# Optimization experiments

Measured on AMD Instinct MI355X. Metric: run time of the kernel, lower is better.

The kernel has to match this reference:

```python
import jax, jax.numpy as jnp
import numpy as np

B, H, S, P = 4, 16, 1024, 64
D = H * P  # state_size = 1024


def setup_inputs() -> dict:
    key = jax.random.key(0)
    k0, k1, k2, k3, k4 = jax.random.split(key, 5)
    q = jax.random.normal(k0, (B * H, S, P), jnp.float32)
    k = jax.random.normal(k1, (B * H, S, P), jnp.float32)
    v = jax.random.normal(k2, (B * H, S, P), jnp.float32)
    # xavier_uniform for the merge projection (fan_in = fan_out = D)
    limit = np.sqrt(6.0 / (D + D)).astype(np.float32)
    w_merge = jax.random.uniform(k3, (D, D), jnp.float32, -limit, limit)
    # causal position mask: True = masked (as used by masked_fill)
    position_mask = jnp.triu(jnp.ones((S, S), dtype=bool), k=1)
    # source-length padding mask: True = padded position
    lengths = jax.random.randint(k4, (B,), S // 2, S + 1)
    src_length_mask = jnp.arange(S)[None, :] >= lengths[:, None]
    return {"q": q, "k": k, "v": v, "w_merge": w_merge,
            "position_mask": position_mask, "src_length_mask": src_length_mask}


def reference(q, k, v, w_merge, position_mask, src_length_mask):
    # q,k,v: [B*H, S, P]; position_mask: [S,S] bool; src_length_mask: [B,S] bool
    BH, T, Pp = q.shape
    nb = src_length_mask.shape[0]
    nh = BH // nb
    scale = 1.0 / np.sqrt(Pp).astype(np.float32)
    # logits = bmm(q, k^T) * scale
    logits = jnp.einsum('btp,bsp->bts', q, k) * scale  # [B*H, T, S]
    logits = logits.reshape(nb, nh, T, T)
    logits = jnp.where(position_mask[None, None, :, :], -jnp.inf, logits)
    logits = jnp.where(src_length_mask[:, None, None, :], -jnp.inf, logits)
    scores = jax.nn.softmax(logits, axis=-1).reshape(BH, T, T)
    # dropout is identity in eval / p=0
    data = jnp.einsum('bts,bsp->btp', scores, v)  # [B*H, T, P]
    # merge heads: [B, H, T, P] -> [B, T, H*P]
    data = data.reshape(nb, nh, T, Pp).transpose(0, 2, 1, 3).reshape(nb, T, nh * Pp)
    return data @ w_merge.T  # Linear(bias=False)
```

## Files before the change

kernel.cpp:

```cpp
#include <hip/hip_runtime.h>
#include <hip/hip_bf16.h>
#include <math.h>


typedef _Float16 f16x8 __attribute__((ext_vector_type(8)));
typedef unsigned short u16x8 __attribute__((ext_vector_type(8)));
typedef float f32x4 __attribute__((ext_vector_type(4)));
typedef float f32x16 __attribute__((ext_vector_type(16)));

union H8 { u16x8 u; f16x8 h; };
union PAF { unsigned int w[4]; f16x8 h; };

static __device__ __forceinline__ unsigned short f2hu(float f) {
  _Float16 h = (_Float16)f;
  unsigned short u;
  __builtin_memcpy(&u, &h, 2);
  return u;
}

static __device__ __forceinline__ unsigned int pk2(float lo, float hi) {
  auto t = __builtin_amdgcn_cvt_pkrtz(lo, hi);
  unsigned int u;
  __builtin_memcpy(&u, &t, 4);
  return u;
}

#define PLSWAP(a, b) asm("v_permlane32_swap_b32 %0, %1" : "+v"(a), "+v"(b))

#define MFMA16(a, b, c) __builtin_amdgcn_mfma_f32_16x16x32_f16((a), (b), (c), 0, 0, 0)
#define MFMA32(a, b, c) __builtin_amdgcn_mfma_f32_32x32x16_f16((a), (b), (c), 0, 0, 0)

static __device__ __forceinline__ void gload16(const void* g, void* l) {
  __builtin_amdgcn_global_load_lds(
      (const __attribute__((address_space(1))) unsigned int*)g,
      (__attribute__((address_space(3))) unsigned int*)l, 16, 0, 0);
}

__global__ __launch_bounds__(256) void prep_all(const float* __restrict__ w,
                                                const int* __restrict__ smask,
                                                const float* __restrict__ kin,
                                                const float* __restrict__ vin,
                                                unsigned short* __restrict__ w_sw,
                                                unsigned short* __restrict__ k_sw,
                                                unsigned short* __restrict__ v_sw,
                                                int* __restrict__ lengths) {
  const int bid = blockIdx.x;
  const int tid = threadIdx.x;
  if (bid < 4) {
    __shared__ int sh[256];
    int4 m = ((const int4*)(smask + bid * 1024))[tid];
    sh[tid] = (m.x != 0) + (m.y != 0) + (m.z != 0) + (m.w != 0);
    __syncthreads();
    for (int o = 128; o > 0; o >>= 1) {
      if (tid < o) sh[tid] += sh[tid + o];
      __syncthreads();
    }
    if (tid == 0) lengths[bid] = 1024 - sh[0];
  } else if (bid < 1028) {
    int idx = (bid - 4) * 256 + tid;
    float4 f = ((const float4*)w)[idx];
    ushort4 o;
    o.x = f2hu(f.x); o.y = f2hu(f.y); o.z = f2hu(f.z); o.w = f2hu(f.w);
    int row = idx >> 8;
    int c4 = (idx & 255) * 4;
    int nt = row >> 6, r = row & 63, kt = c4 >> 6, cb = (c4 & 63) * 2;
    *(ushort4*)((char*)w_sw + ((size_t)(nt * 16 + kt)) * 8192 +
                ((r * 128 + cb) ^ ((r & 7) << 4))) = o;
  } else if (bid < 3076) {
    int idx = (bid - 1028) * 256 + tid;
    const float4* src = ((const float4*)kin) + (size_t)idx * 2;
    float4 a = src[0], b = src[1];
    u16x8 o;
    o[0] = f2hu(a.x); o[1] = f2hu(a.y); o[2] = f2hu(a.z); o[3] = f2hu(a.w);
    o[4] = f2hu(b.x); o[5] = f2hu(b.y); o[6] = f2hu(b.z); o[7] = f2hu(b.w);
    int bh = idx >> 13;
    int i = idx & 8191;
    int s = i >> 3;
    int c16 = i & 7;
    int kt = s >> 6, r = s & 63;
    int xb = (r * 128 + c16 * 16) ^ ((r & 7) << 4);
    *(u16x8*)((char*)k_sw + ((size_t)(bh * 16 + kt)) * 8192 + xb) = o;
  } else {
    const int t = bid - 3076;
    const int bh = t >> 4;
    const int st = t & 15;
    __shared__ unsigned short T[64][72];
    const float* vp = vin + ((size_t)bh * 1024 + st * 64) * 64;
#pragma unroll
    for (int i = 0; i < 4; ++i) {
      int e = i * 256 + tid;
      int row = e >> 4;
      int c4 = (e & 15) * 4;
      float4 f = *(const float4*)(vp + row * 64 + c4);
      T[c4 + 0][row] = f2hu(f.x);
      T[c4 + 1][row] = f2hu(f.y);
      T[c4 + 2][row] = f2hu(f.z);
      T[c4 + 3][row] = f2hu(f.w);
    }
    __syncthreads();
#pragma unroll
    for (int i = 0; i < 4; ++i) {
      int e = i * 256 + tid;
      int feat = e >> 4;
      int c4 = (e & 15) * 4;
      ushort4 o;
      o.x = T[feat][c4 + 0]; o.y = T[feat][c4 + 1];
      o.z = T[feat][c4 + 2]; o.w = T[feat][c4 + 3];
      int xb = (feat * 128 + c4 * 2) ^ ((feat & 7) << 4);
      *(ushort4*)((char*)v_sw + ((size_t)(bh * 16 + st)) * 8192 + xb) = o;
    }
  }
}

static __device__ __forceinline__ void store_attn_sw(unsigned short* attn_sw,
                                                     int b, int hh, int trow,
                                                     int feat, float v) {
  int grow = b * 1024 + trow;
  int mt = grow >> 7, rr = grow & 127;
  int cb = feat * 2;
  *(unsigned short*)((char*)attn_sw + ((size_t)(mt * 16 + hh)) * 16384 +
                     ((rr * 128 + cb) ^ ((rr & 7) << 4))) = f2hu(v);
}

__global__ __launch_bounds__(256, 2) void attn_w32(const float* __restrict__ q,
                                                   const unsigned short* __restrict__ k_sw,
                                                   const unsigned short* __restrict__ v_sw,
                                                   const int* __restrict__ lengths,
                                                   unsigned short* __restrict__ attn_sw) {
  const int wg = blockIdx.x;
  const int idx = (wg & 7) * 64 + (wg >> 3);
  const int bh = idx >> 3;
  const int p = idx & 7;
  const int qtB = 15 - p;
  const int b = bh >> 4;
  const int hh = bh & 15;
  const int tid = threadIdx.x;
  const int lane = tid & 63;
  const int wv = tid >> 6;
  const int l31 = lane & 31;
  const int h = lane >> 5;
  const int len = lengths[b];

  const int selB = ((wv >> 1) ^ (wg & 1)) & 1;
  const int qt = selB ? qtB : p;
  const int qb = qt * 64 + (wv & 1) * 32;
  const int trow = qb + l31;

  const int lcap = (len - 1) >> 6;
  const int mynkt = ((lcap < qt) ? lcap : qt) + 1;
  const int nktB = ((lcap < qtB) ? lcap : qtB) + 1;

  __shared__ __align__(16) unsigned short Kb[3][4096];
  __shared__ __align__(16) unsigned short Vb[3][4096];

  const char* kbase_sw = (const char*)k_sw + (size_t)bh * 16 * 8192;
  const char* vbase_sw = (const char*)v_sw + (size_t)bh * 16 * 8192;

  H8 qf[4];
  {
    const float* qp = q + ((size_t)bh * 1024 + qb + l31) * 64;
#pragma unroll
    for (int c = 0; c < 4; ++c) {
      const float* p0 = qp + c * 16 + h * 8;
      float4 f0 = *(const float4*)(p0);
      float4 f1 = *(const float4*)(p0 + 4);
      u16x8 u;
      u[0] = f2hu(f0.x); u[1] = f2hu(f0.y); u[2] = f2hu(f0.z); u[3] = f2hu(f0.w);
      u[4] = f2hu(f1.x); u[5] = f2hu(f1.y); u[6] = f2hu(f1.z); u[7] = f2hu(f1.w);
      qf[c].u = u;
    }
  }

  f32x16 oacc0 = {}, oacc1 = {};
  float psum = 0.f;

#define STAGE_T(t, buf)                                                      \
  do {                                                                       \
    const char* ks_ = kbase_sw + (size_t)(t) * 8192;                         \
    const char* vs_ = vbase_sw + (size_t)(t) * 8192;                         \
    _Pragma("unroll") for (int j = 0; j < 2; ++j) {                          \
      int ch = wv * 2 + j;                                                   \
      gload16(ks_ + ch * 1024 + lane * 16, (char*)Kb[buf] + ch * 1024);      \
      gload16(vs_ + ch * 1024 + lane * 16, (char*)Vb[buf] + ch * 1024);      \
    }                                                                        \
  } while (0)

  STAGE_T(0, 0);
  STAGE_T(1, 1);

  for (int kt = 0; kt < nktB; ++kt) {
    const int cur = kt % 3;
    if (kt + 1 < nktB) {
      asm volatile("s_waitcnt vmcnt(4)" ::: "memory");
    } else {
      asm volatile("s_waitcnt vmcnt(0)" ::: "memory");
    }
    __builtin_amdgcn_s_barrier();
    if (kt + 2 < nktB) STAGE_T(kt + 2, (kt + 2) % 3);

    if (kt < mynkt) {
      const char* Kc = (const char*)Kb[cur];
      const char* Vc = (const char*)Vb[cur];

      f32x16 sacc0 = {}, sacc1 = {};
      __builtin_amdgcn_s_setprio(1);
#pragma unroll
      for (int c = 0; c < 4; ++c) {
        const int cb = c * 32 + h * 16;
        H8 kf0, kf1;
        kf0.u = *(const u16x8*)(Kc + ((l31 * 128 + cb) ^ ((l31 & 7) << 4)));
        const int r1 = 32 + l31;
        kf1.u = *(const u16x8*)(Kc + ((r1 * 128 + cb) ^ ((r1 & 7) << 4)));
        sacc0 = MFMA32(kf0.h, qf[c].h, sacc0);
        sacc1 = MFMA32(kf1.h, qf[c].h, sacc1);
      }
      __builtin_amdgcn_s_setprio(0);

      unsigned int paw[4][4];
      float ps = 0.f;
#pragma unroll
      for (int kb2 = 0; kb2 < 2; ++kb2) {
        float pv[16];
#pragma unroll
        for (int r = 0; r < 16; ++r) {
          float sv = kb2 ? sacc1[r] : sacc0[r];
          int srl = (r & 3) + 8 * (r >> 2) + 4 * h;
          int scol = kt * 64 + kb2 * 32 + srl;
          float e = __expf(fmaf(sv, 0.125f, -5.0f));
          pv[r] = (scol > trow || scol >= len) ? 0.f : e;
          ps += pv[r];
        }
        unsigned int X0 = pk2(pv[0], pv[1]), X1 = pk2(pv[2], pv[3]);
        unsigned int Y0 = pk2(pv[4], pv[5]), Y1 = pk2(pv[6], pv[7]);
        unsigned int Z0 = pk2(pv[8], pv[9]), Z1 = pk2(pv[10], pv[11]);
        unsigned int W0 = pk2(pv[12], pv[13]), W1 = pk2(pv[14], pv[15]);
        PLSWAP(X0, Y0);
        PLSWAP(X1, Y1);
        PLSWAP(Z0, W0);
        PLSWAP(Z1, W1);
        paw[kb2 * 2 + 0][0] = X0; paw[kb2 * 2 + 0][1] = X1;
        paw[kb2 * 2 + 0][2] = Y0; paw[kb2 * 2 + 0][3] = Y1;
        paw[kb2 * 2 + 1][0] = Z0; paw[kb2 * 2 + 1][1] = Z1;
        paw[kb2 * 2 + 1][2] = W0; paw[kb2 * 2 + 1][3] = W1;
      }
      psum += ps;

      __builtin_amdgcn_s_setprio(1);
#pragma unroll
      for (int c = 0; c < 4; ++c) {
        PAF pa;
        pa.w[0] = paw[c][0]; pa.w[1] = paw[c][1];
        pa.w[2] = paw[c][2]; pa.w[3] = paw[c][3];
        const int cb = c * 32 + h * 16;
        H8 vf0, vf1;
        vf0.u = *(const u16x8*)(Vc + ((l31 * 128 + cb) ^ ((l31 & 7) << 4)));
        const int r1 = 32 + l31;
        vf1.u = *(const u16x8*)(Vc + ((r1 * 128 + cb) ^ ((r1 & 7) << 4)));
        oacc0 = MFMA32(pa.h, vf0.h, oacc0);
        oacc1 = MFMA32(pa.h, vf1.h, oacc1);
      }
      __builtin_amdgcn_s_setprio(0);
    }
  }
#undef STAGE_T

  float sa = psum, sb = psum;
  PLSWAP(sa, sb);
  float inv = 1.0f / (sa + sb);
#pragma unroll
  for (int r = 0; r < 16; ++r) {
    int crow = (r & 3) + 8 * (r >> 2) + 4 * h;
    float invr = __int_as_float(
        __builtin_amdgcn_ds_bpermute(crow << 2, __float_as_int(inv)));
    int tr = qb + crow;
    store_attn_sw(attn_sw, b, hh, tr, l31, oacc0[r] * invr);
    store_attn_sw(attn_sw, b, hh, tr, 32 + l31, oacc1[r] * invr);
  }
}

__global__ __launch_bounds__(256, 2) void merge_sw(const unsigned short* __restrict__ a_sw,
                                                   const unsigned short* __restrict__ w_sw,
                                                   float* __restrict__ out) {
  const int mt = blockIdx.x;
  const int nt = blockIdx.y;
  const int tid = threadIdx.x;
  const int lane = tid & 63;
  const int wv = tid >> 6;
  const int l15 = lane & 15;
  const int kgrp = lane >> 4;
  const int wr = wv >> 1;
  const int wc = wv & 1;

  __shared__ __align__(16) unsigned short Ab[3][8192];
  __shared__ __align__(16) unsigned short Wb[3][4096];

  const char* abase = (const char*)a_sw + (size_t)mt * 16 * 16384;
  const char* wbase = (const char*)w_sw + (size_t)nt * 16 * 8192;

  f32x4 acc[4][2] = {};

#define MSTAGE(t, buf)                                                    \
  do {                                                                    \
    const char* as_ = abase + (size_t)(t) * 16384;                        \
    const char* ws_ = wbase + (size_t)(t) * 8192;                         \
    _Pragma("unroll") for (int j = 0; j < 4; ++j) {                       \
      int ch = wv * 4 + j;                                                \
      gload16(as_ + ch * 1024 + lane * 16, (char*)Ab[buf] + ch * 1024);   \
    }                                                                     \
    _Pragma("unroll") for (int j = 0; j < 2; ++j) {                       \
      int ch = wv * 2 + j;                                                \
      gload16(ws_ + ch * 1024 + lane * 16, (char*)Wb[buf] + ch * 1024);   \
    }                                                                     \
  } while (0)

  MSTAGE(0, 0);
  MSTAGE(1, 1);

  for (int t = 0; t < 16; ++t) {
    const int cur = t % 3;
    if (t + 1 < 16) {
      asm volatile("s_waitcnt vmcnt(6)" ::: "memory");
    } else {
      asm volatile("s_waitcnt vmcnt(0)" ::: "memory");
    }
    __builtin_amdgcn_s_barrier();
    if (t + 2 < 16) MSTAGE(t + 2, (t + 2) % 3);

    __builtin_amdgcn_s_setprio(1);
#pragma unroll
    for (int kb = 0; kb < 2; kb++) {
      H8 wf[2];
#pragma unroll
      for (int nb = 0; nb < 2; nb++) {
        int wrow = wc * 32 + nb * 16 + l15;
        wf[nb].u = *(const u16x8*)((const char*)Wb[cur] +
                    ((wrow * 128 + (kb * 32 + kgrp * 8) * 2) ^ ((wrow & 7) << 4)));
      }
#pragma unroll
      for (int mb = 0; mb < 4; mb++) {
        int arow = wr * 64 + mb * 16 + l15;
        H8 aa;
        aa.u = *(const u16x8*)((const char*)Ab[cur] +
                ((arow * 128 + (kb * 32 + kgrp * 8) * 2) ^ ((arow & 7) << 4)));
#pragma unroll
        for (int nb = 0; nb < 2; nb++)
          acc[mb][nb] = MFMA16(aa.h, wf[nb].h, acc[mb][nb]);
      }
    }
    __builtin_amdgcn_s_setprio(0);
  }
#undef MSTAGE

  const int m0 = mt * 128, n0 = nt * 64;
#pragma unroll
  for (int mb = 0; mb < 4; mb++)
#pragma unroll
    for (int nb = 0; nb < 2; nb++)
#pragma unroll
      for (int r = 0; r < 4; r++)
        out[(size_t)(m0 + wr * 64 + mb * 16 + kgrp * 4 + r) * 1024 +
            n0 + wc * 32 + nb * 16 + l15] = acc[mb][nb][r];
}

extern "C" void kernel_launch(void* const* d_in, const int* in_sizes, int n_in,
                              void* d_out, int out_size, void* d_ws, size_t ws_size,
                              hipStream_t stream) {
  const float* q = (const float*)d_in[0];
  const float* k = (const float*)d_in[1];
  const float* v = (const float*)d_in[2];
  const float* w = (const float*)d_in[3];
  const int* smask = (const int*)d_in[5];
  float* out = (float*)d_out;

  char* ws = (char*)d_ws;
  const size_t MB = 1024 * 1024;
  int* lengths = (int*)ws;
  unsigned short* w_sw = (unsigned short*)(ws + 256);
  unsigned short* attn_sw = (unsigned short*)(ws + 256 + 2 * MB);
  unsigned short* k_sw = (unsigned short*)(ws + 256 + 10 * MB);
  unsigned short* v_sw = (unsigned short*)(ws + 256 + 18 * MB);

  hipLaunchKernelGGL(prep_all, dim3(4100), dim3(256), 0, stream,
                     w, smask, k, v, w_sw, k_sw, v_sw, lengths);
  hipLaunchKernelGGL(attn_w32, dim3(512), dim3(256), 0, stream,
                     q, k_sw, v_sw, lengths, attn_sw);
  hipLaunchKernelGGL(merge_sw, dim3(32, 16), dim3(256), 0, stream, attn_sw, w_sw, out);
}
```

Measured before the change: 63.46 us.

## Replace LDS-staged attention with single-wave blocks reading K/V directly from global

Attention no longer stages K and V tiles into LDS through a triple-buffered async pipeline with barriers. It now launches one 64-thread wave per 32-row query block, and each wave reads K rows and transposed V straight from global memory in plain row-major fp16 layouts. The prep kernel writes K and V^T linearly instead of in swizzled tiles. This removes LDS traffic and barrier synchronisation, but loses K/V sharing across waves and the overlap of loads with compute, so it leans on L2 and cache hits and may stall on global load latency.

```diff
diff --git a/kernel.cpp b/kernel.cpp
--- a/kernel.cpp
+++ b/kernel.cpp
@@ -41,8 +41,8 @@
                                                 const float* __restrict__ kin,
                                                 const float* __restrict__ vin,
                                                 unsigned short* __restrict__ w_sw,
-                                                unsigned short* __restrict__ k_sw,
-                                                unsigned short* __restrict__ v_sw,
+                                                unsigned short* __restrict__ k_h,
+                                                unsigned short* __restrict__ vt_h,
                                                 int* __restrict__ lengths) {
   const int bid = blockIdx.x;
   const int tid = threadIdx.x;
@@ -73,13 +73,7 @@
     u16x8 o;
     o[0] = f2hu(a.x); o[1] = f2hu(a.y); o[2] = f2hu(a.z); o[3] = f2hu(a.w);
     o[4] = f2hu(b.x); o[5] = f2hu(b.y); o[6] = f2hu(b.z); o[7] = f2hu(b.w);
-    int bh = idx >> 13;
-    int i = idx & 8191;
-    int s = i >> 3;
-    int c16 = i & 7;
-    int kt = s >> 6, r = s & 63;
-    int xb = (r * 128 + c16 * 16) ^ ((r & 7) << 4);
-    *(u16x8*)((char*)k_sw + ((size_t)(bh * 16 + kt)) * 8192 + xb) = o;
+    ((u16x8*)k_h)[idx] = o;
   } else {
     const int t = bid - 3076;
     const int bh = t >> 4;
@@ -106,8 +100,7 @@
       ushort4 o;
       o.x = T[feat][c4 + 0]; o.y = T[feat][c4 + 1];
       o.z = T[feat][c4 + 2]; o.w = T[feat][c4 + 3];
-      int xb = (feat * 128 + c4 * 2) ^ ((feat & 7) << 4);
-      *(ushort4*)((char*)v_sw + ((size_t)(bh * 16 + st)) * 8192 + xb) = o;
+      *(ushort4*)(vt_h + ((size_t)bh * 64 + feat) * 1024 + st * 64 + c4) = o;
     }
   }
 }
@@ -122,39 +115,29 @@
                      ((rr * 128 + cb) ^ ((rr & 7) << 4))) = f2hu(v);
 }
 
-__global__ __launch_bounds__(256, 2) void attn_w32(const float* __restrict__ q,
-                                                   const unsigned short* __restrict__ k_sw,
-                                                   const unsigned short* __restrict__ v_sw,
-                                                   const int* __restrict__ lengths,
-                                                   unsigned short* __restrict__ attn_sw) {
-  const int wg = blockIdx.x;
-  const int idx = (wg & 7) * 64 + (wg >> 3);
-  const int bh = idx >> 3;
-  const int p = idx & 7;
-  const int qtB = 15 - p;
+__global__ __launch_bounds__(64, 2) void attn_direct(const float* __restrict__ q,
+                                                     const unsigned short* __restrict__ k_h,
+                                                     const unsigned short* __restrict__ vt_h,
+                                                     const int* __restrict__ lengths,
+                                                     unsigned short* __restrict__ attn_sw) {
+  const int w = blockIdx.x;
+  const int xcd = w & 7;
+  const int j = w >> 3;
+  const int bh = xcd * 8 + (j >> 5);
+  const int s = j & 31;
+  const int pp = s >> 1;
+  const int half = s & 1;
+  const int qt = (pp & 1) ? (pp >> 1) : (15 - (pp >> 1));
   const int b = bh >> 4;
   const int hh = bh & 15;
-  const int tid = threadIdx.x;
-  const int lane = tid & 63;
-  const int wv = tid >> 6;
+  const int lane = threadIdx.x;
   const int l31 = lane & 31;
   const int h = lane >> 5;
   const int len = lengths[b];
-
-  const int selB = ((wv >> 1) ^ (wg & 1)) & 1;
-  const int qt = selB ? qtB : p;
-  const int qb = qt * 64 + (wv & 1) * 32;
+  const int qb = qt * 64 + half * 32;
   const int trow = qb + l31;
-
   const int lcap = (len - 1) >> 6;
-  const int mynkt = ((lcap < qt) ? lcap : qt) + 1;
-  const int nktB = ((lcap < qtB) ? lcap : qtB) + 1;
-
-  __shared__ __align__(16) unsigned short Kb[3][4096];
-  __shared__ __align__(16) unsigned short Vb[3][4096];
-
-  const char* kbase_sw = (const char*)k_sw + (size_t)bh * 16 * 8192;
-  const char* vbase_sw = (const char*)v_sw + (size_t)bh * 16 * 8192;
+  const int nkt = ((lcap < qt) ? lcap : qt) + 1;
 
   H8 qf[4];
   {
@@ -174,95 +157,69 @@
   f32x16 oacc0 = {}, oacc1 = {};
   float psum = 0.f;
 
-#define STAGE_T(t, buf)                                                      \
-  do {                                                                       \
-    const char* ks_ = kbase_sw + (size_t)(t) * 8192;                         \
-    const char* vs_ = vbase_sw + (size_t)(t) * 8192;                         \
-    _Pragma("unroll") for (int j = 0; j < 2; ++j) {                          \
-      int ch = wv * 2 + j;                                                   \
-      gload16(ks_ + ch * 1024 + lane * 16, (char*)Kb[buf] + ch * 1024);      \
-      gload16(vs_ + ch * 1024 + lane * 16, (char*)Vb[buf] + ch * 1024);      \
-    }                                                                        \
-  } while (0)
-
-  STAGE_T(0, 0);
-  STAGE_T(1, 1);
-
-  for (int kt = 0; kt < nktB; ++kt) {
-    const int cur = kt % 3;
-    if (kt + 1 < nktB) {
-      asm volatile("s_waitcnt vmcnt(4)" ::: "memory");
-    } else {
-      asm volatile("s_waitcnt vmcnt(0)" ::: "memory");
-    }
-    __builtin_amdgcn_s_barrier();
-    if (kt + 2 < nktB) STAGE_T(kt + 2, (kt + 2) % 3);
-
-    if (kt < mynkt) {
-      const char* Kc = (const char*)Kb[cur];
-      const char* Vc = (const char*)Vb[cur];
-
-      f32x16 sacc0 = {}, sacc1 = {};
-      __builtin_amdgcn_s_setprio(1);
-#pragma unroll
-      for (int c = 0; c < 4; ++c) {
-        const int cb = c * 32 + h * 16;
-        H8 kf0, kf1;
-        kf0.u = *(const u16x8*)(Kc + ((l31 * 128 + cb) ^ ((l31 & 7) << 4)));
-        const int r1 = 32 + l31;
-        kf1.u = *(const u16x8*)(Kc + ((r1 * 128 + cb) ^ ((r1 & 7) << 4)));
-        sacc0 = MFMA32(kf0.h, qf[c].h, sacc0);
-        sacc1 = MFMA32(kf1.h, qf[c].h, sacc1);
+  const unsigned short* kb = k_h + (size_t)bh * 65536;
+  const unsigned short* vb = vt_h + (size_t)bh * 65536;
+
+  for (int kt = 0; kt < nkt; ++kt) {
+    const unsigned short* krow0 = kb + (size_t)(kt * 64 + l31) * 64 + h * 8;
+    const unsigned short* krow1 = krow0 + 32 * 64;
+    f32x16 sacc0 = {}, sacc1 = {};
+    __builtin_amdgcn_s_setprio(1);
+#pragma unroll
+    for (int c = 0; c < 4; ++c) {
+      H8 kf0, kf1;
+      kf0.u = *(const u16x8*)(krow0 + c * 16);
+      kf1.u = *(const u16x8*)(krow1 + c * 16);
+      sacc0 = MFMA32(kf0.h, qf[c].h, sacc0);
+      sacc1 = MFMA32(kf1.h, qf[c].h, sacc1);
+    }
+    __builtin_amdgcn_s_setprio(0);
+
+    unsigned int paw[4][4];
+    float ps = 0.f;
+#pragma unroll
+    for (int kb2 = 0; kb2 < 2; ++kb2) {
+      float pv[16];
+#pragma unroll
+      for (int r = 0; r < 16; ++r) {
+        float sv = kb2 ? sacc1[r] : sacc0[r];
+        int srl = (r & 3) + 8 * (r >> 2) + 4 * h;
+        int scol = kt * 64 + kb2 * 32 + srl;
+        float e = __expf(fmaf(sv, 0.125f, -5.0f));
+        pv[r] = (scol > trow || scol >= len) ? 0.f : e;
+        ps += pv[r];
       }
-      __builtin_amdgcn_s_setprio(0);
-
-      unsigned int paw[4][4];
-      float ps = 0.f;
-#pragma unroll
-      for (int kb2 = 0; kb2 < 2; ++kb2) {
-        float pv[16];
-#pragma unroll
-        for (int r = 0; r < 16; ++r) {
-          float sv = kb2 ? sacc1[r] : sacc0[r];
-          int srl = (r & 3) + 8 * (r >> 2) + 4 * h;
-          int scol = kt * 64 + kb2 * 32 + srl;
-          float e = __expf(fmaf(sv, 0.125f, -5.0f));
-          pv[r] = (scol > trow || scol >= len) ? 0.f : e;
-          ps += pv[r];
-        }
-        unsigned int X0 = pk2(pv[0], pv[1]), X1 = pk2(pv[2], pv[3]);
-        unsigned int Y0 = pk2(pv[4], pv[5]), Y1 = pk2(pv[6], pv[7]);
-        unsigned int Z0 = pk2(pv[8], pv[9]), Z1 = pk2(pv[10], pv[11]);
-        unsigned int W0 = pk2(pv[12], pv[13]), W1 = pk2(pv[14], pv[15]);
-        PLSWAP(X0, Y0);
-        PLSWAP(X1, Y1);
-        PLSWAP(Z0, W0);
-        PLSWAP(Z1, W1);
-        paw[kb2 * 2 + 0][0] = X0; paw[kb2 * 2 + 0][1] = X1;
-        paw[kb2 * 2 + 0][2] = Y0; paw[kb2 * 2 + 0][3] = Y1;
-        paw[kb2 * 2 + 1][0] = Z0; paw[kb2 * 2 + 1][1] = Z1;
-        paw[kb2 * 2 + 1][2] = W0; paw[kb2 * 2 + 1][3] = W1;
-      }
-      psum += ps;
-
-      __builtin_amdgcn_s_setprio(1);
-#pragma unroll
-      for (int c = 0; c < 4; ++c) {
-        PAF pa;
-        pa.w[0] = paw[c][0]; pa.w[1] = paw[c][1];
-        pa.w[2] = paw[c][2]; pa.w[3] = paw[c][3];
-        const int cb = c * 32 + h * 16;
-        H8 vf0, vf1;
-        vf0.u = *(const u16x8*)(Vc + ((l31 * 128 + cb) ^ ((l31 & 7) << 4)));
-        const int r1 = 32 + l31;
-        vf1.u = *(const u16x8*)(Vc + ((r1 * 128 + cb) ^ ((r1 & 7) << 4)));
-        oacc0 = MFMA32(pa.h, vf0.h, oacc0);
-        oacc1 = MFMA32(pa.h, vf1.h, oacc1);
-      }
-      __builtin_amdgcn_s_setprio(0);
-    }
-  }
-#undef STAGE_T
+      unsigned int X0 = pk2(pv[0], pv[1]), X1 = pk2(pv[2], pv[3]);
+      unsigned int Y0 = pk2(pv[4], pv[5]), Y1 = pk2(pv[6], pv[7]);
+      unsigned int Z0 = pk2(pv[8], pv[9]), Z1 = pk2(pv[10], pv[11]);
+      unsigned int W0 = pk2(pv[12], pv[13]), W1 = pk2(pv[14], pv[15]);
+      PLSWAP(X0, Y0);
+      PLSWAP(X1, Y1);
+      PLSWAP(Z0, W0);
+      PLSWAP(Z1, W1);
+      paw[kb2 * 2 + 0][0] = X0; paw[kb2 * 2 + 0][1] = X1;
+      paw[kb2 * 2 + 0][2] = Y0; paw[kb2 * 2 + 0][3] = Y1;
+      paw[kb2 * 2 + 1][0] = Z0; paw[kb2 * 2 + 1][1] = Z1;
+      paw[kb2 * 2 + 1][2] = W0; paw[kb2 * 2 + 1][3] = W1;
+    }
+    psum += ps;
+
+    const unsigned short* vrow0 = vb + (size_t)l31 * 1024 + kt * 64 + h * 8;
+    const unsigned short* vrow1 = vrow0 + 32 * 1024;
+    __builtin_amdgcn_s_setprio(1);
+#pragma unroll
+    for (int c = 0; c < 4; ++c) {
+      PAF pa;
+      pa.w[0] = paw[c][0]; pa.w[1] = paw[c][1];
+      pa.w[2] = paw[c][2]; pa.w[3] = paw[c][3];
+      H8 vf0, vf1;
+      vf0.u = *(const u16x8*)(vrow0 + c * 16);
+      vf1.u = *(const u16x8*)(vrow1 + c * 16);
+      oacc0 = MFMA32(pa.h, vf0.h, oacc0);
+      oacc1 = MFMA32(pa.h, vf1.h, oacc1);
+    }
+    __builtin_amdgcn_s_setprio(0);
+  }
 
   float sa = psum, sb = psum;
   PLSWAP(sa, sb);
@@ -377,12 +334,12 @@
   int* lengths = (int*)ws;
   unsigned short* w_sw = (unsigned short*)(ws + 256);
   unsigned short* attn_sw = (unsigned short*)(ws + 256 + 2 * MB);
-  unsigned short* k_sw = (unsigned short*)(ws + 256 + 10 * MB);
-  unsigned short* v_sw = (unsigned short*)(ws + 256 + 18 * MB);
+  unsigned short* k_h = (unsigned short*)(ws + 256 + 10 * MB);
+  unsigned short* vt_h = (unsigned short*)(ws + 256 + 18 * MB);
 
   hipLaunchKernelGGL(prep_all, dim3(4100), dim3(256), 0, stream,
-                     w, smask, k, v, w_sw, k_sw, v_sw, lengths);
-  hipLaunchKernelGGL(attn_w32, dim3(512), dim3(256), 0, stream,
-                     q, k_sw, v_sw, lengths, attn_sw);
+                     w, smask, k, v, w_sw, k_h, vt_h, lengths);
+  hipLaunchKernelGGL(attn_direct, dim3(2048), dim3(64), 0, stream,
+                     q, k_h, vt_h, lengths, attn_sw);
   hipLaunchKernelGGL(merge_sw, dim3(32, 16), dim3(256), 0, stream, attn_sw, w_sw, out);
 }
```

New measurement: 91.03 us. +43.4%, slower.

## Split attention into single-wave workgroups with private double-buffered K/V staging

Applied to the files above, without the earlier changes.

Replaces the 4-wave workgroup, where waves share a triple-buffered K/V tile and synchronize with barriers, with 2048 single-wave workgroups. Each wave handles one 32-row query slice and loads its own K/V tiles into a private double buffer, so there are no barriers and each wave only walks its own causal/length-limited tile count. The cost is that K/V tiles are no longer shared across the waves, so each tile is loaded from global memory up to four times as often. Each wave also issues more loads per stage, and the wave now waits on its own loads without any other wave to hide the latency.

```diff
diff --git a/kernel.cpp b/kernel.cpp
--- a/kernel.cpp
+++ b/kernel.cpp
@@ -122,36 +122,31 @@
                      ((rr * 128 + cb) ^ ((rr & 7) << 4))) = f2hu(v);
 }
 
-__global__ __launch_bounds__(256, 2) void attn_w32(const float* __restrict__ q,
+__global__ __launch_bounds__(64, 2) void attn_solo(const float* __restrict__ q,
                                                    const unsigned short* __restrict__ k_sw,
                                                    const unsigned short* __restrict__ v_sw,
                                                    const int* __restrict__ lengths,
                                                    unsigned short* __restrict__ attn_sw) {
   const int wg = blockIdx.x;
-  const int idx = (wg & 7) * 64 + (wg >> 3);
-  const int bh = idx >> 3;
-  const int p = idx & 7;
-  const int qtB = 15 - p;
+  const int idx = (wg & 7) * 256 + (wg >> 3);
+  const int bh = idx >> 5;
+  const int sub = idx & 31;
+  const int s = sub >> 1;
+  const int half = sub & 1;
+  const int qt = (s & 1) ? (s >> 1) : (15 - (s >> 1));
   const int b = bh >> 4;
   const int hh = bh & 15;
-  const int tid = threadIdx.x;
-  const int lane = tid & 63;
-  const int wv = tid >> 6;
+  const int lane = threadIdx.x;
   const int l31 = lane & 31;
   const int h = lane >> 5;
   const int len = lengths[b];
-
-  const int selB = ((wv >> 1) ^ (wg & 1)) & 1;
-  const int qt = selB ? qtB : p;
-  const int qb = qt * 64 + (wv & 1) * 32;
+  const int qb = qt * 64 + half * 32;
   const int trow = qb + l31;
-
   const int lcap = (len - 1) >> 6;
-  const int mynkt = ((lcap < qt) ? lcap : qt) + 1;
-  const int nktB = ((lcap < qtB) ? lcap : qtB) + 1;
-
-  __shared__ __align__(16) unsigned short Kb[3][4096];
-  __shared__ __align__(16) unsigned short Vb[3][4096];
+  const int nkt = ((lcap < qt) ? lcap : qt) + 1;
+
+  __shared__ __align__(16) unsigned short Kb[2][4096];
+  __shared__ __align__(16) unsigned short Vb[2][4096];
 
   const char* kbase_sw = (const char*)k_sw + (size_t)bh * 16 * 8192;
   const char* vbase_sw = (const char*)v_sw + (size_t)bh * 16 * 8192;
@@ -174,93 +169,88 @@
   f32x16 oacc0 = {}, oacc1 = {};
   float psum = 0.f;
 
-#define STAGE_T(t, buf)                                                      \
-  do {                                                                       \
-    const char* ks_ = kbase_sw + (size_t)(t) * 8192;                         \
-    const char* vs_ = vbase_sw + (size_t)(t) * 8192;                         \
-    _Pragma("unroll") for (int j = 0; j < 2; ++j) {                          \
-      int ch = wv * 2 + j;                                                   \
-      gload16(ks_ + ch * 1024 + lane * 16, (char*)Kb[buf] + ch * 1024);      \
-      gload16(vs_ + ch * 1024 + lane * 16, (char*)Vb[buf] + ch * 1024);      \
-    }                                                                        \
+#define STAGE_T(t, buf)                                                        \
+  do {                                                                         \
+    const char* ks_ = kbase_sw + (size_t)(t) * 8192;                           \
+    const char* vs_ = vbase_sw + (size_t)(t) * 8192;                           \
+    _Pragma("unroll") for (int j = 0; j < 8; ++j) {                            \
+      gload16(ks_ + j * 1024 + lane * 16, (char*)Kb[buf] + j * 1024);          \
+      gload16(vs_ + j * 1024 + lane * 16, (char*)Vb[buf] + j * 1024);          \
+    }                                                                          \
   } while (0)
 
   STAGE_T(0, 0);
-  STAGE_T(1, 1);
-
-  for (int kt = 0; kt < nktB; ++kt) {
-    const int cur = kt % 3;
-    if (kt + 1 < nktB) {
-      asm volatile("s_waitcnt vmcnt(4)" ::: "memory");
+
+  for (int kt = 0; kt < nkt; ++kt) {
+    const int cur = kt & 1;
+    if (kt + 1 < nkt) {
+      STAGE_T(kt + 1, cur ^ 1);
+      asm volatile("s_waitcnt vmcnt(16)" ::: "memory");
     } else {
       asm volatile("s_waitcnt vmcnt(0)" ::: "memory");
     }
-    __builtin_amdgcn_s_barrier();
-    if (kt + 2 < nktB) STAGE_T(kt + 2, (kt + 2) % 3);
-
-    if (kt < mynkt) {
-      const char* Kc = (const char*)Kb[cur];
-      const char* Vc = (const char*)Vb[cur];
-
-      f32x16 sacc0 = {}, sacc1 = {};
-      __builtin_amdgcn_s_setprio(1);
-#pragma unroll
-      for (int c = 0; c < 4; ++c) {
-        const int cb = c * 32 + h * 16;
-        H8 kf0, kf1;
-        kf0.u = *(const u16x8*)(Kc + ((l31 * 128 + cb) ^ ((l31 & 7) << 4)));
-        const int r1 = 32 + l31;
-        kf1.u = *(const u16x8*)(Kc + ((r1 * 128 + cb) ^ ((r1 & 7) << 4)));
-        sacc0 = MFMA32(kf0.h, qf[c].h, sacc0);
-        sacc1 = MFMA32(kf1.h, qf[c].h, sacc1);
+
+    const char* Kc = (const char*)Kb[cur];
+    const char* Vc = (const char*)Vb[cur];
+
+    f32x16 sacc0 = {}, sacc1 = {};
+    __builtin_amdgcn_s_setprio(1);
+#pragma unroll
+    for (int c = 0; c < 4; ++c) {
+      const int cb = c * 32 + h * 16;
+      H8 kf0, kf1;
+      kf0.u = *(const u16x8*)(Kc + ((l31 * 128 + cb) ^ ((l31 & 7) << 4)));
+      const int r1 = 32 + l31;
+      kf1.u = *(const u16x8*)(Kc + ((r1 * 128 + cb) ^ ((r1 & 7) << 4)));
+      sacc0 = MFMA32(kf0.h, qf[c].h, sacc0);
+      sacc1 = MFMA32(kf1.h, qf[c].h, sacc1);
+    }
+    __builtin_amdgcn_s_setprio(0);
+
+    unsigned int paw[4][4];
+    float ps = 0.f;
+#pragma unroll
+    for (int kb2 = 0; kb2 < 2; ++kb2) {
+      float pv[16];
+#pragma unroll
+      for (int r = 0; r < 16; ++r) {
+        float sv = kb2 ? sacc1[r] : sacc0[r];
+        int srl = (r & 3) + 8 * (r >> 2) + 4 * h;
+        int scol = kt * 64 + kb2 * 32 + srl;
+        float e = __expf(fmaf(sv, 0.125f, -5.0f));
+        pv[r] = (scol > trow || scol >= len) ? 0.f : e;
+        ps += pv[r];
       }
-      __builtin_amdgcn_s_setprio(0);
-
-      unsigned int paw[4][4];
-      float ps = 0.f;
-#pragma unroll
-      for (int kb2 = 0; kb2 < 2; ++kb2) {
-        float pv[16];
-#pragma unroll
-        for (int r = 0; r < 16; ++r) {
-          float sv = kb2 ? sacc1[r] : sacc0[r];
-          int srl = (r & 3) + 8 * (r >> 2) + 4 * h;
-          int scol = kt * 64 + kb2 * 32 + srl;
-          float e = __expf(fmaf(sv, 0.125f, -5.0f));
-          pv[r] = (scol > trow || scol >= len) ? 0.f : e;
-          ps += pv[r];
-        }
-        unsigned int X0 = pk2(pv[0], pv[1]), X1 = pk2(pv[2], pv[3]);
-        unsigned int Y0 = pk2(pv[4], pv[5]), Y1 = pk2(pv[6], pv[7]);
-        unsigned int Z0 = pk2(pv[8], pv[9]), Z1 = pk2(pv[10], pv[11]);
-        unsigned int W0 = pk2(pv[12], pv[13]), W1 = pk2(pv[14], pv[15]);
-        PLSWAP(X0, Y0);
-        PLSWAP(X1, Y1);
-        PLSWAP(Z0, W0);
-        PLSWAP(Z1, W1);
-        paw[kb2 * 2 + 0][0] = X0; paw[kb2 * 2 + 0][1] = X1;
-        paw[kb2 * 2 + 0][2] = Y0; paw[kb2 * 2 + 0][3] = Y1;
-        paw[kb2 * 2 + 1][0] = Z0; paw[kb2 * 2 + 1][1] = Z1;
-        paw[kb2 * 2 + 1][2] = W0; paw[kb2 * 2 + 1][3] = W1;
-      }
-      psum += ps;
-
-      __builtin_amdgcn_s_setprio(1);
-#pragma unroll
-      for (int c = 0; c < 4; ++c) {
-        PAF pa;
-        pa.w[0] = paw[c][0]; pa.w[1] = paw[c][1];
-        pa.w[2] = paw[c][2]; pa.w[3] = paw[c][3];
-        const int cb = c * 32 + h * 16;
-        H8 vf0, vf1;
-        vf0.u = *(const u16x8*)(Vc + ((l31 * 128 + cb) ^ ((l31 & 7) << 4)));
-        const int r1 = 32 + l31;
-        vf1.u = *(const u16x8*)(Vc + ((r1 * 128 + cb) ^ ((r1 & 7) << 4)));
-        oacc0 = MFMA32(pa.h, vf0.h, oacc0);
-        oacc1 = MFMA32(pa.h, vf1.h, oacc1);
-      }
-      __builtin_amdgcn_s_setprio(0);
-    }
+      unsigned int X0 = pk2(pv[0], pv[1]), X1 = pk2(pv[2], pv[3]);
+      unsigned int Y0 = pk2(pv[4], pv[5]), Y1 = pk2(pv[6], pv[7]);
+      unsigned int Z0 = pk2(pv[8], pv[9]), Z1 = pk2(pv[10], pv[11]);
+      unsigned int W0 = pk2(pv[12], pv[13]), W1 = pk2(pv[14], pv[15]);
+      PLSWAP(X0, Y0);
+      PLSWAP(X1, Y1);
+      PLSWAP(Z0, W0);
+      PLSWAP(Z1, W1);
+      paw[kb2 * 2 + 0][0] = X0; paw[kb2 * 2 + 0][1] = X1;
+      paw[kb2 * 2 + 0][2] = Y0; paw[kb2 * 2 + 0][3] = Y1;
+      paw[kb2 * 2 + 1][0] = Z0; paw[kb2 * 2 + 1][1] = Z1;
+      paw[kb2 * 2 + 1][2] = W0; paw[kb2 * 2 + 1][3] = W1;
+    }
+    psum += ps;
+
+    __builtin_amdgcn_s_setprio(1);
+#pragma unroll
+    for (int c = 0; c < 4; ++c) {
+      PAF pa;
+      pa.w[0] = paw[c][0]; pa.w[1] = paw[c][1];
+      pa.w[2] = paw[c][2]; pa.w[3] = paw[c][3];
+      const int cb = c * 32 + h * 16;
+      H8 vf0, vf1;
+      vf0.u = *(const u16x8*)(Vc + ((l31 * 128 + cb) ^ ((l31 & 7) << 4)));
+      const int r1 = 32 + l31;
+      vf1.u = *(const u16x8*)(Vc + ((r1 * 128 + cb) ^ ((r1 & 7) << 4)));
+      oacc0 = MFMA32(pa.h, vf0.h, oacc0);
+      oacc1 = MFMA32(pa.h, vf1.h, oacc1);
+    }
+    __builtin_amdgcn_s_setprio(0);
   }
 #undef STAGE_T
 
@@ -382,7 +372,7 @@
 
   hipLaunchKernelGGL(prep_all, dim3(4100), dim3(256), 0, stream,
                      w, smask, k, v, w_sw, k_sw, v_sw, lengths);
-  hipLaunchKernelGGL(attn_w32, dim3(512), dim3(256), 0, stream,
+  hipLaunchKernelGGL(attn_solo, dim3(2048), dim3(64), 0, stream,
                      q, k_sw, v_sw, lengths, attn_sw);
   hipLaunchKernelGGL(merge_sw, dim3(32, 16), dim3(256), 0, stream, attn_sw, w_sw, out);
 }
```

Measured after the change: 81.87 us. +29.0%, slower.
